# Kernel optimization log

Measured on AMD Instinct MI355X. Metric: run time of the kernel, lower is better.

## Reference

```python
import jax, jax.numpy as jnp
import numpy as np


def setup_inputs() -> dict:
    key = jax.random.key(0)
    k_x, k_w0, k_w1 = jax.random.split(key, 3)
    x = jax.random.normal(k_x, (1, 48, 56, 56), dtype=jnp.float32)   # kjml
    w0 = jax.random.normal(k_w0, (96, 9), dtype=jnp.float32)          # weights[0]
    w1 = jax.random.normal(k_w1, (48, 9), dtype=jnp.float32)          # weights[1]
    return {"x": x, "w0": w0, "w1": w1}


def reference(x, w0, w1):
    # t_3: [k=1, j=48, l=56, m=56, i=9]
    t3 = jnp.einsum('kjml,ji->kjlmi', x, w1)
    # reshape j=48 -> (n=2, g=24), sum over g -> [1, 2, 56, 56, 9]
    t4 = t3.reshape(1, 2, 24, 56, 56, 9).sum(axis=2)
    # t_5: [k=1, n=2, j=96, l=56, m=56]
    t5 = jnp.einsum('knlmi,ji->knjlm', t4, w0)
    # merge (n=2, j=96) -> 192 channels
    return t5.reshape(1, 192, 56, 56)
```

## Files before the change

### kernel.cpp

```cpp
#include <hip/hip_runtime.h>


#define S    56
#define SP   3136
#define G    24
#define LB   4
#define JB   12

__global__ __launch_bounds__(256)
void conv_mix_fused(const float* __restrict__ x, const float* __restrict__ w0,
                    const float* __restrict__ w1, float* __restrict__ out) {
    __shared__ float xs[G * LB * S];
    __shared__ float Wl[JB * G];
    const int l0  = blockIdx.x * LB;
    const int j0  = blockIdx.y * JB;
    const int n   = blockIdx.z;
    const int tid = threadIdx.x;

    for (int idx = tid; idx < JB * G; idx += 256) {
        int j = idx / G, g = idx % G;
        float s = 0.f;
        #pragma unroll
        for (int i = 0; i < 9; ++i)
            s += w0[(j0 + j) * 9 + i] * w1[(n * G + g) * 9 + i];
        Wl[idx] = s;
    }

    const float* xn = x + n * G * SP;
    #pragma unroll
    for (int it = 0; it < (G * LB * S) / 256; ++it) {
        int idx = it * 256 + tid;
        int ll = idx & (LB - 1);
        int m  = (idx >> 2) % S;
        int g  = idx / (LB * S);
        xs[(g * LB + ll) * S + m] = xn[g * SP + m * S + l0 + ll];
    }
    __syncthreads();

    if (tid < LB * S) {
        const int ll = tid / S;
        const int m  = tid % S;
        float xv[G];
        #pragma unroll
        for (int g = 0; g < G; ++g)
            xv[g] = xs[(g * LB + ll) * S + m];

        const int l = l0 + ll;
        float* orow = out + (size_t)(n * 96 + j0) * SP + l * S + m;
        #pragma unroll
        for (int j = 0; j < JB; ++j) {
            float acc = 0.f;
            #pragma unroll
            for (int g = 0; g < G; ++g)
                acc += Wl[j * G + g] * xv[g];
            orow[j * SP] = acc;
        }
    }
}

extern "C" void kernel_launch(void* const* d_in, const int* in_sizes, int n_in,
                              void* d_out, int out_size, void* d_ws, size_t ws_size,
                              hipStream_t stream) {
    const float* x  = (const float*)d_in[0];
    const float* w0 = (const float*)d_in[1];
    const float* w1 = (const float*)d_in[2];
    float* out = (float*)d_out;
    (void)d_ws; (void)ws_size;

    dim3 grid(S / LB, 96 / JB, 2);
    conv_mix_fused<<<grid, 256, 0, stream>>>(x, w0, w1, out);
}
```

Before: 61.17 us.

## Load input directly as float4 into registers and split output channels across thread groups

Drops the shared-memory staging of the transposed input. Each thread now loads float4 vectors of 4 consecutive l values per g straight into registers, issued before the weight precompute so the loads can overlap it. The output channel work is also split across 4 thread groups of 3 channels each, so all 224 active threads handle different j instead of each thread computing all 12. This reduces shared-memory traffic and per-thread serial work, but raises register pressure (96 floats for xv) and makes the global loads strided by row rather than coalesced.

```diff
diff --git a/kernel.cpp b/kernel.cpp
--- a/kernel.cpp
+++ b/kernel.cpp
@@ -4,56 +4,60 @@
 #define S    56
 #define SP   3136
 #define G    24
-#define LB   4
 #define JB   12
+#define JPT  3
 
 __global__ __launch_bounds__(256)
 void conv_mix_fused(const float* __restrict__ x, const float* __restrict__ w0,
                     const float* __restrict__ w1, float* __restrict__ out) {
-    __shared__ float xs[G * LB * S];
     __shared__ float Wl[JB * G];
-    const int l0  = blockIdx.x * LB;
+    const int bx  = blockIdx.x;
     const int j0  = blockIdx.y * JB;
     const int n   = blockIdx.z;
     const int tid = threadIdx.x;
 
+    const int  m      = tid % S;
+    const int  jq     = tid / S;
+    const bool active = tid < 4 * S;
+
+    float4 xv[G];
+    if (active) {
+        const float4* x4 = reinterpret_cast<const float4*>(x)
+                         + (size_t)n * G * (SP / 4) + m * (S / 4) + bx;
+        #pragma unroll
+        for (int g = 0; g < G; ++g)
+            xv[g] = x4[g * (SP / 4)];
+    }
+
     for (int idx = tid; idx < JB * G; idx += 256) {
-        int j = idx / G, g = idx % G;
+        int j = idx / G, g = idx - j * G;
         float s = 0.f;
         #pragma unroll
         for (int i = 0; i < 9; ++i)
             s += w0[(j0 + j) * 9 + i] * w1[(n * G + g) * 9 + i];
         Wl[idx] = s;
     }
-
-    const float* xn = x + n * G * SP;
-    #pragma unroll
-    for (int it = 0; it < (G * LB * S) / 256; ++it) {
-        int idx = it * 256 + tid;
-        int ll = idx & (LB - 1);
-        int m  = (idx >> 2) % S;
-        int g  = idx / (LB * S);
-        xs[(g * LB + ll) * S + m] = xn[g * SP + m * S + l0 + ll];
-    }
     __syncthreads();
 
-    if (tid < LB * S) {
-        const int ll = tid / S;
-        const int m  = tid % S;
-        float xv[G];
+    if (active) {
+        float* obase = out + (size_t)(n * 96 + j0 + jq * JPT) * SP
+                     + (bx * 4) * S + m;
         #pragma unroll
-        for (int g = 0; g < G; ++g)
-            xv[g] = xs[(g * LB + ll) * S + m];
-
-        const int l = l0 + ll;
-        float* orow = out + (size_t)(n * 96 + j0) * SP + l * S + m;
-        #pragma unroll
-        for (int j = 0; j < JB; ++j) {
-            float acc = 0.f;
+        for (int j = 0; j < JPT; ++j) {
+            float ax = 0.f, ay = 0.f, az = 0.f, aw = 0.f;
             #pragma unroll
-            for (int g = 0; g < G; ++g)
-                acc += Wl[j * G + g] * xv[g];
-            orow[j * SP] = acc;
+            for (int g = 0; g < G; ++g) {
+                float w = Wl[(jq * JPT + j) * G + g];
+                ax += w * xv[g].x;
+                ay += w * xv[g].y;
+                az += w * xv[g].z;
+                aw += w * xv[g].w;
+            }
+            float* o = obase + j * SP;
+            o[0]     = ax;
+            o[S]     = ay;
+            o[2 * S] = az;
+            o[3 * S] = aw;
         }
     }
 }
@@ -67,6 +71,6 @@
     float* out = (float*)d_out;
     (void)d_ws; (void)ws_size;
 
-    dim3 grid(S / LB, 96 / JB, 2);
+    dim3 grid(S / 4, 96 / JB, 2);
     conv_mix_fused<<<grid, 256, 0, stream>>>(x, w0, w1, out);
 }
```

Result: slower. 62.99 us (+3.0%).
